# Kernel optimization log

Hardware: AMD Instinct MI355X
Metric: run time of the kernel (lower is better)

Reference implementation:

```python
import jax, jax.numpy as jnp
import numpy as np

V, D, H, L, S_MAX, FF = 32000, 1024, 16, 6, 1024, 4096
HD = D // H
EPS = 1e-5

def _ln(x, g, b):
    mu = jnp.mean(x, axis=-1, keepdims=True)
    var = jnp.mean((x - mu) ** 2, axis=-1, keepdims=True)
    return (x - mu) * jax.lax.rsqrt(var + EPS) * g + b

def setup_inputs() -> dict:
    key = jax.random.key(0)
    ks = jax.random.split(key, 12)
    std = 0.02
    d = {}
    d['x'] = jax.random.randint(ks[0], (2, 1024), 0, V)
    d['tok_emb'] = std * jax.random.normal(ks[1], (V, D), jnp.float32)
    d['pos_emb'] = std * jax.random.normal(ks[2], (S_MAX, D), jnp.float32)
    d['ln1_g'] = jnp.ones((L, D)); d['ln1_b'] = jnp.zeros((L, D))
    d['qkv_w'] = std * jax.random.normal(ks[3], (L, 3 * D, D), jnp.float32)
    d['qkv_b'] = jnp.zeros((L, 3 * D))
    d['proj_w'] = std * jax.random.normal(ks[4], (L, D, D), jnp.float32)
    d['proj_b'] = jnp.zeros((L, D))
    d['ln2_g'] = jnp.ones((L, D)); d['ln2_b'] = jnp.zeros((L, D))
    d['fc1_w'] = std * jax.random.normal(ks[5], (L, FF, D), jnp.float32)
    d['fc1_b'] = jnp.zeros((L, FF))
    d['fc2_w'] = std * jax.random.normal(ks[6], (L, D, FF), jnp.float32)
    d['fc2_b'] = jnp.zeros((L, D))
    d['lnf_g'] = jnp.ones((D,)); d['lnf_b'] = jnp.zeros((D,))
    d['head_w'] = std * jax.random.normal(ks[7], (V, D), jnp.float32)
    return d

def _gpt(x, tok_emb, pos_emb, ln1_g, ln1_b, qkv_w, qkv_b, proj_w, proj_b,
         ln2_g, ln2_b, fc1_w, fc1_b, fc2_w, fc2_b, lnf_g, lnf_b, head_w):
    B, S = x.shape
    h = tok_emb[x] + pos_emb[:S][None]  # (B,S,D)
    scale = HD ** -0.5
    causal = jnp.tril(jnp.ones((S, S), bool))
    neg_inf = jnp.finfo(h.dtype).min

    def block(h, p):
        l1g, l1b, qw, qb, pw, pb, l2g, l2b, f1w, f1b, f2w, f2b = p
        xn = _ln(h, l1g, l1b)
        qkv = xn @ qw.T + qb  # (B,S,3D)
        qkv = qkv.reshape(B, S, 3, H, HD).transpose(2, 0, 3, 1, 4)  # (3,B,H,S,HD)
        q, k, v = qkv[0], qkv[1], qkv[2]
        scores = jnp.einsum('bhqd,bhkd->bhqk', q, k) * scale
        scores = jnp.where(causal, scores, neg_inf)
        attn = jax.nn.softmax(scores, axis=-1)
        o = jnp.einsum('bhqk,bhkd->bhqd', attn, v)
        o = o.transpose(0, 2, 1, 3).reshape(B, S, D)
        h = h + (o @ pw.T + pb)
        xn = _ln(h, l2g, l2b)
        ff = jax.nn.gelu(xn @ f1w.T + f1b, approximate=False) @ f2w.T + f2b
        return h + ff, None

    params = (ln1_g, ln1_b, qkv_w, qkv_b, proj_w, proj_b,
              ln2_g, ln2_b, fc1_w, fc1_b, fc2_w, fc2_b)
    h, _ = jax.lax.scan(block, h, params)
    h = _ln(h, lnf_g, lnf_b)
    return h @ head_w.T  # (B,S,V)

def reference(x, tok_emb, pos_emb, ln1_g, ln1_b, qkv_w, qkv_b, proj_w, proj_b,
              ln2_g, ln2_b, fc1_w, fc1_b, fc2_w, fc2_b, lnf_g, lnf_b, head_w):
    return _gpt(x, tok_emb, pos_emb, ln1_g, ln1_b, qkv_w, qkv_b, proj_w, proj_b,
                ln2_g, ln2_b, fc1_w, fc1_b, fc2_w, fc2_b, lnf_g, lnf_b, head_w)
```

## Files before the change

### kernel.cpp

```cpp
#include <hip/hip_runtime.h>

typedef unsigned short u16;
typedef unsigned int   u32;
typedef __bf16 bf16x8 __attribute__((ext_vector_type(8)));
typedef float  f32x4  __attribute__((ext_vector_type(4)));

#define DEV __device__ __forceinline__

DEV u16 f2bf(float f) {
    u32 u = __builtin_bit_cast(u32, f);
    u32 r = u + 0x7FFFu + ((u >> 16) & 1u);
    return (u16)(r >> 16);
}

DEV void gload16(const void* g, void* l) {
    __builtin_amdgcn_global_load_lds((const __attribute__((address_space(1))) void*)g,
                                     (__attribute__((address_space(3))) void*)l, 16, 0, 0);
}

DEV int xcd_swz(int bid, int nwg) {
    int q = nwg >> 3, r = nwg & 7;
    int xcd = bid & 7, idx = bid >> 3;
    return (xcd < r ? xcd * (q + 1) : r * (q + 1) + (xcd - r) * q) + idx;
}

DEV int swz(int p) {
    int m = (((p >> 7) & 1) << 6) | (((p >> 9) & 1) << 5) | (((p >> 8) & 1) << 4);
    return p ^ m;
}

__global__ void cvt_k(const float* __restrict__ src, u16* __restrict__ dst, int n4) {
    int i = blockIdx.x * blockDim.x + threadIdx.x;
    int stride = gridDim.x * blockDim.x;
    for (; i < n4; i += stride) {
        float4 v = ((const float4*)src)[i];
        ushort4 u;
        u.x = f2bf(v.x); u.y = f2bf(v.y); u.z = f2bf(v.z); u.w = f2bf(v.w);
        ((ushort4*)dst)[i] = u;
    }
}

__global__ void cvt4_k(const float* __restrict__ s0, const float* __restrict__ s1,
                       const float* __restrict__ s2, const float* __restrict__ s3,
                       u16* __restrict__ dst, int n0, int n1, int n2, int n3) {
    int i = blockIdx.x * blockDim.x + threadIdx.x;
    int stride = gridDim.x * blockDim.x;
    int t0 = n0, t1 = t0 + n1, t2 = t1 + n2, t3 = t2 + n3;
    for (; i < t3; i += stride) {
        const float* s; int j;
        if (i < t0)      { s = s0; j = i; }
        else if (i < t1) { s = s1; j = i - t0; }
        else if (i < t2) { s = s2; j = i - t1; }
        else             { s = s3; j = i - t2; }
        float4 v = ((const float4*)s)[j];
        ushort4 u;
        u.x = f2bf(v.x); u.y = f2bf(v.y); u.z = f2bf(v.z); u.w = f2bf(v.w);
        ((ushort4*)dst)[i] = u;
    }
}

DEV void ln_store(float4 v, const float* __restrict__ g, const float* __restrict__ b,
                  u16* __restrict__ out, int row, int t) {
    float s = v.x + v.y + v.z + v.w;
    float s2 = v.x * v.x + v.y * v.y + v.z * v.z + v.w * v.w;
    #pragma unroll
    for (int msk = 1; msk < 64; msk <<= 1) {
        s  += __shfl_xor(s, msk);
        s2 += __shfl_xor(s2, msk);
    }
    __shared__ float ps[4], ps2[4];
    if ((t & 63) == 0) { ps[t >> 6] = s; ps2[t >> 6] = s2; }
    __syncthreads();
    s = ps[0] + ps[1] + ps[2] + ps[3];
    s2 = ps2[0] + ps2[1] + ps2[2] + ps2[3];
    float mu = s * (1.0f / 1024.0f);
    float var = s2 * (1.0f / 1024.0f) - mu * mu;
    float rstd = rsqrtf(var + 1e-5f);
    float4 gg = ((const float4*)g)[t];
    float4 bb = ((const float4*)b)[t];
    ushort4 o;
    o.x = f2bf((v.x - mu) * rstd * gg.x + bb.x);
    o.y = f2bf((v.y - mu) * rstd * gg.y + bb.y);
    o.z = f2bf((v.z - mu) * rstd * gg.z + bb.z);
    o.w = f2bf((v.w - mu) * rstd * gg.w + bb.w);
    ((ushort4*)out)[(size_t)row * 256 + t] = o;
}

__global__ void ln_k(const float* __restrict__ in, const float* __restrict__ g,
                     const float* __restrict__ b, u16* __restrict__ out) {
    int row = blockIdx.x;
    int t = threadIdx.x;
    float4 v = ((const float4*)(in + (size_t)row * 1024))[t];
    ln_store(v, g, b, out, row, t);
}

__global__ void embed_ln_k(const int* __restrict__ x, const float* __restrict__ te,
                           const float* __restrict__ pe, float* __restrict__ h,
                           const float* __restrict__ g, const float* __restrict__ b,
                           u16* __restrict__ xn) {
    int row = blockIdx.x;
    int t = threadIdx.x;
    int tok = x[row];
    int s = row & 1023;
    float4 a = ((const float4*)(te + (size_t)tok * 1024))[t];
    float4 p = ((const float4*)(pe + (size_t)s * 1024))[t];
    a.x += p.x; a.y += p.y; a.z += p.z; a.w += p.w;
    ((float4*)(h + (size_t)row * 1024))[t] = a;
    ln_store(a, g, b, xn, row, t);
}

__global__ void fuse2ln_k(const float* __restrict__ p0, const float* __restrict__ p1,
                          const float* __restrict__ bias, float* __restrict__ h,
                          const float* __restrict__ g, const float* __restrict__ b,
                          u16* __restrict__ xn) {
    int row = blockIdx.x;
    int t = threadIdx.x;
    size_t idx = (size_t)row * 256 + t;
    float4 a = ((const float4*)p0)[idx];
    float4 bb = ((const float4*)p1)[idx];
    float4 c = ((const float4*)bias)[t];
    float4 v = ((const float4*)h)[idx];
    v.x += a.x + bb.x + c.x;
    v.y += a.y + bb.y + c.y;
    v.z += a.z + bb.z + c.z;
    v.w += a.w + bb.w + c.w;
    ((float4*)h)[idx] = v;
    ln_store(v, g, b, xn, row, t);
}

template<int PH>
DEV void phase_mma(const bf16x8 (&af)[2][2], const bf16x8 (&bfr)[4][2], f32x4 (&acc)[8][4]) {
    __builtin_amdgcn_s_barrier();
    asm volatile("s_waitcnt lgkmcnt(0)" ::: "memory");
    __builtin_amdgcn_sched_barrier(0);
    __builtin_amdgcn_s_setprio(1);
    #pragma unroll
    for (int ms = 0; ms < 2; ++ms)
        #pragma unroll
        for (int nj = 0; nj < 4; ++nj)
            #pragma unroll
            for (int kk = 0; kk < 2; ++kk)
                acc[PH * 2 + ms][nj] = __builtin_amdgcn_mfma_f32_16x16x32_bf16(
                    af[ms][kk], bfr[nj][kk], acc[PH * 2 + ms][nj], 0, 0, 0);
    __builtin_amdgcn_s_setprio(0);
}

template<int PH>
DEV void read_afrags(const char* Ab, int arow, int fr, int fq, bf16x8 (&af)[2][2]) {
    #pragma unroll
    for (int ms = 0; ms < 2; ++ms)
        #pragma unroll
        for (int kk = 0; kk < 2; ++kk) {
            int lin = (arow + (PH * 2 + ms) * 16 + fr) * 128 + kk * 64 + fq * 16;
            af[ms][kk] = *(const bf16x8*)(Ab + swz(lin));
        }
}

template<int BIAS, int OUTBF>
__global__ __launch_bounds__(512, 2)
void gemm8p(const u16* __restrict__ A, const u16* __restrict__ Bw,
            const float* __restrict__ bias,
            float* __restrict__ outf, u16* __restrict__ outb,
            int M, int N, int K) {
    __shared__ char lds[131072];
    char* ldsA = lds;
    char* ldsB = lds + 65536;
    const int t = threadIdx.x;
    const int w = t >> 6, l = t & 63;
    const int fr = l & 15, fq = l >> 4;
    const int wm = w >> 2, wn = w & 3;

    int bid = blockIdx.y * gridDim.x + blockIdx.x;
    int swzb = xcd_swz(bid, gridDim.x * gridDim.y);
    const int m0 = (swzb % gridDim.x) * 256;
    const int n0 = (swzb / gridDim.x) * 256;
    const int nt = K >> 6;
    const int arow = wm * 128;

    const u16* Asrc = A + (size_t)m0 * K;
    const u16* Bsrc = Bw + (size_t)n0 * K;

    size_t o00, o01, o10, o11;
    {
        int p;
        p = 0 * 16384 + 0 * 8192 + t * 16; o00 = (size_t)(p >> 7) * K + ((swz(p) & 127) >> 1);
        p = 0 * 16384 + 1 * 8192 + t * 16; o01 = (size_t)(p >> 7) * K + ((swz(p) & 127) >> 1);
        p = 1 * 16384 + 0 * 8192 + t * 16; o10 = (size_t)(p >> 7) * K + ((swz(p) & 127) >> 1);
        p = 1 * 16384 + 1 * 8192 + t * 16; o11 = (size_t)(p >> 7) * K + ((swz(p) & 127) >> 1);
    }
    const int wb = w * 1024;

    gload16(Asrc + o00, ldsA + wb);
    gload16(Asrc + o01, ldsA + 8192 + wb);
    gload16(Asrc + o10, ldsA + 16384 + wb);
    gload16(Asrc + o11, ldsA + 16384 + 8192 + wb);
    gload16(Bsrc + o00, ldsB + wb);
    gload16(Bsrc + o01, ldsB + 8192 + wb);
    gload16(Bsrc + o10, ldsB + 16384 + wb);
    gload16(Bsrc + o11, ldsB + 16384 + 8192 + wb);
    gload16(Bsrc + o00 + 64, ldsB + 32768 + wb);
    gload16(Bsrc + o01 + 64, ldsB + 32768 + 8192 + wb);
    gload16(Bsrc + o10 + 64, ldsB + 32768 + 16384 + wb);
    gload16(Bsrc + o11 + 64, ldsB + 32768 + 16384 + 8192 + wb);
    asm volatile("s_waitcnt vmcnt(4)" ::: "memory");
    __builtin_amdgcn_s_barrier();
    __builtin_amdgcn_sched_barrier(0);

    f32x4 acc[8][4] = {};

    for (int T = 0; T < nt; ++T) {
        const char* Ab = ldsA + (T & 1) * 32768;
        const char* Bb = ldsB + (T & 1) * 32768;
        char* Anx = ldsA + ((T + 1) & 1) * 32768;
        char* Bnx = ldsB + (T & 1) * 32768;
        const bool stA = (T + 1 < nt), stB = (T + 2 < nt);
        const size_t kA = (size_t)(T + 1) * 64, kB = (size_t)(T + 2) * 64;

        bf16x8 bfr[4][2], af[2][2];

        #pragma unroll
        for (int nj = 0; nj < 4; ++nj)
            #pragma unroll
            for (int kk = 0; kk < 2; ++kk) {
                int lin = (wn * 64 + nj * 16 + fr) * 128 + kk * 64 + fq * 16;
                bfr[nj][kk] = *(const bf16x8*)(Bb + swz(lin));
            }
        read_afrags<0>(Ab, arow, fr, fq, af);
        if (stA) {
            gload16(Asrc + o00 + kA, Anx + wb);
            gload16(Asrc + o01 + kA, Anx + 8192 + wb);
        }
        phase_mma<0>(af, bfr, acc);
        __builtin_amdgcn_s_barrier();

        read_afrags<1>(Ab, arow, fr, fq, af);
        if (stA) {
            gload16(Asrc + o10 + kA, Anx + 16384 + wb);
            gload16(Asrc + o11 + kA, Anx + 16384 + 8192 + wb);
        }
        phase_mma<1>(af, bfr, acc);
        __builtin_amdgcn_s_barrier();

        read_afrags<2>(Ab, arow, fr, fq, af);
        if (stB) {
            gload16(Bsrc + o00 + kB, Bnx + wb);
            gload16(Bsrc + o01 + kB, Bnx + 8192 + wb);
        }
        phase_mma<2>(af, bfr, acc);
        __builtin_amdgcn_s_barrier();

        read_afrags<3>(Ab, arow, fr, fq, af);
        if (stB) {
            gload16(Bsrc + o10 + kB, Bnx + 16384 + wb);
            gload16(Bsrc + o11 + kB, Bnx + 16384 + 8192 + wb);
        }
        phase_mma<3>(af, bfr, acc);
        if (stB)      asm volatile("s_waitcnt vmcnt(4)" ::: "memory");
        else if (stA) asm volatile("s_waitcnt vmcnt(0)" ::: "memory");
        __builtin_amdgcn_s_barrier();
        __builtin_amdgcn_sched_barrier(0);
    }

    #pragma unroll
    for (int mi = 0; mi < 8; ++mi) {
        #pragma unroll
        for (int nj = 0; nj < 4; ++nj) {
            #pragma unroll
            for (int r = 0; r < 4; ++r) {
                int row = m0 + wm * 128 + mi * 16 + fq * 4 + r;
                int col = n0 + wn * 64 + nj * 16 + fr;
                float v = acc[mi][nj][r];
                if (BIAS) v += bias[col];
                if (OUTBF) outb[(size_t)row * N + col] = f2bf(v);
                else       outf[(size_t)row * N + col] = v;
            }
        }
    }
}

template<int BIAS, int GELU_, int OUTBF, int SPLITK>
__global__ __launch_bounds__(512, 2)
void gemm4p(const u16* __restrict__ A, const u16* __restrict__ Bw,
            const float* __restrict__ bias,
            float* __restrict__ outf, u16* __restrict__ outb,
            int M, int N, int K) {
    __shared__ char lds[65536];
    char* ldsA = lds;
    char* ldsB = lds + 32768;
    const int t = threadIdx.x;
    const int w = t >> 6, l = t & 63;
    const int fr = l & 15, fq = l >> 4;
    const int wm = w >> 2, wn = w & 3;

    int bid = blockIdx.y * gridDim.x + blockIdx.x;
    int swzb = xcd_swz(bid, gridDim.x * gridDim.y);
    const int m0 = (swzb % gridDim.x) * 128;
    const int n0 = (swzb / gridDim.x) * 128;

    int kbase = 0, Keff = K;
    if (SPLITK) { Keff = K >> 1; kbase = blockIdx.z * Keff; }
    const int nt = Keff >> 6;

    const u16* Asrc = A + (size_t)m0 * K + kbase;
    const u16* Bsrc = Bw + (size_t)n0 * K + kbase;

    size_t o0, o1;
    {
        int p = t * 16;        o0 = (size_t)(p >> 7) * K + ((swz(p) & 127) >> 1);
        p = 8192 + t * 16;     o1 = (size_t)(p >> 7) * K + ((swz(p) & 127) >> 1);
    }
    const int wb = w * 1024;

    gload16(Asrc + o0, ldsA + wb);
    gload16(Asrc + o1, ldsA + 8192 + wb);
    gload16(Bsrc + o0, ldsB + wb);
    gload16(Bsrc + o1, ldsB + 8192 + wb);
    gload16(Bsrc + o0 + 64, ldsB + 16384 + wb);
    gload16(Bsrc + o1 + 64, ldsB + 16384 + 8192 + wb);
    asm volatile("s_waitcnt vmcnt(2)" ::: "memory");
    __builtin_amdgcn_s_barrier();
    __builtin_amdgcn_sched_barrier(0);

    f32x4 acc[4][2] = {};

    for (int T = 0; T < nt; ++T) {
        const char* Ab = ldsA + (T & 1) * 16384;
        const char* Bb = ldsB + (T & 1) * 16384;
        char* Anx = ldsA + ((T + 1) & 1) * 16384;
        char* Bnx = ldsB + (T & 1) * 16384;
        const bool stA = (T + 1 < nt), stB = (T + 2 < nt);
        const size_t kA = (size_t)(T + 1) * 64, kB = (size_t)(T + 2) * 64;

        bf16x8 bfr[2][2], af[2][2];

        #pragma unroll
        for (int nj = 0; nj < 2; ++nj)
            #pragma unroll
            for (int kk = 0; kk < 2; ++kk) {
                int lin = (wn * 32 + nj * 16 + fr) * 128 + kk * 64 + fq * 16;
                bfr[nj][kk] = *(const bf16x8*)(Bb + swz(lin));
            }
        #pragma unroll
        for (int ms = 0; ms < 2; ++ms)
            #pragma unroll
            for (int kk = 0; kk < 2; ++kk) {
                int lin = (wm * 64 + ms * 16 + fr) * 128 + kk * 64 + fq * 16;
                af[ms][kk] = *(const bf16x8*)(Ab + swz(lin));
            }
        if (stA) {
            gload16(Asrc + o0 + kA, Anx + wb);
            gload16(Asrc + o1 + kA, Anx + 8192 + wb);
        }
        __builtin_amdgcn_s_barrier();
        asm volatile("s_waitcnt lgkmcnt(0)" ::: "memory");
        __builtin_amdgcn_sched_barrier(0);
        __builtin_amdgcn_s_setprio(1);
        #pragma unroll
        for (int ms = 0; ms < 2; ++ms)
            #pragma unroll
            for (int nj = 0; nj < 2; ++nj)
                #pragma unroll
                for (int kk = 0; kk < 2; ++kk)
                    acc[ms][nj] = __builtin_amdgcn_mfma_f32_16x16x32_bf16(
                        af[ms][kk], bfr[nj][kk], acc[ms][nj], 0, 0, 0);
        __builtin_amdgcn_s_setprio(0);
        __builtin_amdgcn_s_barrier();

        #pragma unroll
        for (int ms = 0; ms < 2; ++ms)
            #pragma unroll
            for (int kk = 0; kk < 2; ++kk) {
                int lin = (wm * 64 + (2 + ms) * 16 + fr) * 128 + kk * 64 + fq * 16;
                af[ms][kk] = *(const bf16x8*)(Ab + swz(lin));
            }
        if (stB) {
            gload16(Bsrc + o0 + kB, Bnx + wb);
            gload16(Bsrc + o1 + kB, Bnx + 8192 + wb);
        }
        __builtin_amdgcn_s_barrier();
        asm volatile("s_waitcnt lgkmcnt(0)" ::: "memory");
        __builtin_amdgcn_sched_barrier(0);
        __builtin_amdgcn_s_setprio(1);
        #pragma unroll
        for (int ms = 0; ms < 2; ++ms)
            #pragma unroll
            for (int nj = 0; nj < 2; ++nj)
                #pragma unroll
                for (int kk = 0; kk < 2; ++kk)
                    acc[2 + ms][nj] = __builtin_amdgcn_mfma_f32_16x16x32_bf16(
                        af[ms][kk], bfr[nj][kk], acc[2 + ms][nj], 0, 0, 0);
        __builtin_amdgcn_s_setprio(0);
        if (stB)      asm volatile("s_waitcnt vmcnt(2)" ::: "memory");
        else if (stA) asm volatile("s_waitcnt vmcnt(0)" ::: "memory");
        __builtin_amdgcn_s_barrier();
        __builtin_amdgcn_sched_barrier(0);
    }

    float* op = outf;
    if (SPLITK) op = outf + (size_t)blockIdx.z * M * N;

    #pragma unroll
    for (int mi = 0; mi < 4; ++mi) {
        #pragma unroll
        for (int nj = 0; nj < 2; ++nj) {
            #pragma unroll
            for (int r = 0; r < 4; ++r) {
                int row = m0 + wm * 64 + mi * 16 + fq * 4 + r;
                int col = n0 + wn * 32 + nj * 16 + fr;
                float v = acc[mi][nj][r];
                if (BIAS) v += bias[col];
                if (GELU_) v = 0.5f * v * (1.0f + erff(v * 0.70710678118f));
                if (OUTBF) outb[(size_t)row * N + col] = f2bf(v);
                else       op[(size_t)row * N + col] = v;
            }
        }
    }
}

template<int BM, int BN, int BIAS, int GELU_, int RES, int OUTBF, int SPLITK>
__global__ void gemm_db(const u16* __restrict__ A, const u16* __restrict__ Bw,
                        const float* __restrict__ bias, const float* __restrict__ res,
                        float* __restrict__ outf, u16* __restrict__ outb,
                        int M, int N, int K) {
    constexpr int MR = BM / 32;
    constexpr int NR = BN / 32;
    constexpr int AL = BM / 64;
    constexpr int BL = BN / 64;
    __shared__ u16 lA[2][BM * 32];
    __shared__ u16 lB[2][BN * 32];
    const int t = threadIdx.x;
    const int w = t >> 6, l = t & 63;

    int bid = blockIdx.y * gridDim.x + blockIdx.x;
    int swzb = xcd_swz(bid, gridDim.x * gridDim.y);
    const int m0 = (swzb % gridDim.x) * BM;
    const int n0 = (swzb / gridDim.x) * BN;

    int kbase = 0, Keff = K;
    if (SPLITK) { Keff = K >> 1; kbase = blockIdx.z * Keff; }
    const int nt = Keff >> 5;

    const int wr = (w >> 1) * (BM / 2), wc = (w & 1) * (BN / 2);
    const int fr = l & 15, fq = l >> 4;
    const int g0 = w * 64 + l;

    const int srow = g0 >> 2, scol = (g0 & 3) * 8;

    f32x4 acc[MR][NR] = {};

    #pragma unroll
    for (int i = 0; i < AL; ++i)
        gload16(A + (size_t)(m0 + srow + i * 64) * K + kbase + scol, lA[0] + (srow + i * 64) * 32 + scol);
    #pragma unroll
    for (int i = 0; i < BL; ++i)
        gload16(Bw + (size_t)(n0 + srow + i * 64) * K + kbase + scol, lB[0] + (srow + i * 64) * 32 + scol);
    __syncthreads();

    for (int T = 0; T < nt; ++T) {
        const int cur = T & 1, nxt = cur ^ 1;
        if (T + 1 < nt) {
            const int kk = kbase + (T + 1) * 32;
            #pragma unroll
            for (int i = 0; i < AL; ++i)
                gload16(A + (size_t)(m0 + srow + i * 64) * K + kk + scol, lA[nxt] + (srow + i * 64) * 32 + scol);
            #pragma unroll
            for (int i = 0; i < BL; ++i)
                gload16(Bw + (size_t)(n0 + srow + i * 64) * K + kk + scol, lB[nxt] + (srow + i * 64) * 32 + scol);
        }
        bf16x8 af[MR], bfv[NR];
        #pragma unroll
        for (int mi = 0; mi < MR; ++mi)
            af[mi] = *(const bf16x8*)(lA[cur] + (wr + mi * 16 + fr) * 32 + fq * 8);
        #pragma unroll
        for (int ni = 0; ni < NR; ++ni)
            bfv[ni] = *(const bf16x8*)(lB[cur] + (wc + ni * 16 + fr) * 32 + fq * 8);
        #pragma unroll
        for (int mi = 0; mi < MR; ++mi)
            #pragma unroll
            for (int ni = 0; ni < NR; ++ni)
                acc[mi][ni] = __builtin_amdgcn_mfma_f32_16x16x32_bf16(af[mi], bfv[ni], acc[mi][ni], 0, 0, 0);
        __syncthreads();
    }

    float* op = outf;
    if (SPLITK) op = outf + (size_t)blockIdx.z * M * N;

    #pragma unroll
    for (int mi = 0; mi < MR; ++mi) {
        #pragma unroll
        for (int ni = 0; ni < NR; ++ni) {
            #pragma unroll
            for (int r = 0; r < 4; ++r) {
                int row = m0 + wr + mi * 16 + fq * 4 + r;
                int col = n0 + wc + ni * 16 + fr;
                float v = acc[mi][ni][r];
                if (BIAS) v += bias[col];
                if (GELU_) v = 0.5f * v * (1.0f + erff(v * 0.70710678118f));
                if (RES) v += res[(size_t)row * N + col];
                if (OUTBF) outb[(size_t)row * N + col] = f2bf(v);
                else       op[(size_t)row * N + col] = v;
            }
        }
    }
}

__global__ __launch_bounds__(512, 2)
void attn_k(const u16* __restrict__ qkv, u16* __restrict__ o) {
    __shared__ u16 lK[64 * 64];
    __shared__ u16 lV[64 * 64];
    __shared__ u16 lP[8 * 16 * 64];
    const int t = threadIdx.x;
    const int w = t >> 6, l = t & 63;
    const int fr = l & 15, fq = l >> 4;

    int swzb = xcd_swz(blockIdx.x, gridDim.x);
    const int qb = 7 - (swzb & 7);
    const int hh = (swzb >> 3) & 15;
    const int b  = swzb >> 7;
    const int q0 = qb * 128;
    const int qw = q0 + w * 16;

    const u16* srcK;
    {
        int p = t * 16;
        int L = swz(p);
        srcK = qkv + ((size_t)(b * 1024) + (L >> 7)) * 3072 + 1024 + hh * 64 + ((L & 127) >> 1);
    }

    const int kvp = (t & 31) * 2;
    const int vd0 = (t >> 5) * 4;
    const u16* srcV = qkv + (size_t)(b * 1024) * 3072 + 2048 + hh * 64 + vd0;

    bf16x8 qf[2];
    {
        size_t base = ((size_t)(b * 1024) + qw + fr) * 3072 + hh * 64;
        qf[0] = *(const bf16x8*)(qkv + base + fq * 8);
        qf[1] = *(const bf16x8*)(qkv + base + 32 + fq * 8);
    }

    float m_run[4], l_run[4];
    f32x4 acc_o[4] = {};
    #pragma unroll
    for (int r = 0; r < 4; ++r) { m_run[r] = -__builtin_inff(); l_run[r] = 0.0f; }

    uint2 gv0 = *(const uint2*)(srcV + (size_t)kvp * 3072);
    uint2 gv1 = *(const uint2*)(srcV + (size_t)(kvp + 1) * 3072);

    const int kv_end = q0 + 128;
    for (int kv0 = 0; kv0 < kv_end; kv0 += 64) {
        #pragma unroll
        for (int j = 0; j < 4; ++j) {
            u32 lo = (j < 2) ? gv0.x : gv0.y;
            u32 hi = (j < 2) ? gv1.x : gv1.y;
            lo = (j & 1) ? (lo >> 16) : (lo & 0xffffu);
            hi = (j & 1) ? (hi >> 16) : (hi & 0xffffu);
            u32 word = lo | (hi << 16);
            int pv = (vd0 + j) * 128 + kvp * 2;
            *(u32*)((char*)lV + swz(pv)) = word;
        }
        gload16(srcK + (size_t)kv0 * 3072, (char*)lK + w * 1024);
        __syncthreads();

        if (kv0 + 64 < kv_end) {
            gv0 = *(const uint2*)(srcV + (size_t)(kv0 + 64 + kvp) * 3072);
            gv1 = *(const uint2*)(srcV + (size_t)(kv0 + 64 + kvp + 1) * 3072);
        }

        const bool active = (kv0 <= qw + 15);
        if (active) {
            f32x4 accs[4] = {};
            #pragma unroll
            for (int nt = 0; nt < 4; ++nt) {
                #pragma unroll
                for (int ks = 0; ks < 2; ++ks) {
                    int pk = ((nt * 16 + fr) * 64 + ks * 32 + fq * 8) * 2;
                    bf16x8 kf = *(const bf16x8*)((const char*)lK + swz(pk));
                    accs[nt] = __builtin_amdgcn_mfma_f32_16x16x32_bf16(qf[ks], kf, accs[nt], 0, 0, 0);
                }
            }

            float p[4][4], mx[4], rs[4];
            #pragma unroll
            for (int r = 0; r < 4; ++r) {
                int qg = qw + fq * 4 + r;
                float m = -__builtin_inff();
                #pragma unroll
                for (int nt = 0; nt < 4; ++nt) {
                    int kvg = kv0 + nt * 16 + fr;
                    float s = (kvg <= qg) ? accs[nt][r] * 0.125f : -__builtin_inff();
                    p[nt][r] = s;
                    m = fmaxf(m, s);
                }
                mx[r] = m;
            }
            #pragma unroll
            for (int msk = 1; msk < 16; msk <<= 1) {
                #pragma unroll
                for (int r = 0; r < 4; ++r) mx[r] = fmaxf(mx[r], __shfl_xor(mx[r], msk));
            }
            float mnew[4], alpha[4];
            #pragma unroll
            for (int r = 0; r < 4; ++r) {
                mnew[r] = fmaxf(m_run[r], mx[r]);
                alpha[r] = __expf(m_run[r] - mnew[r]);
                float s = 0.0f;
                #pragma unroll
                for (int nt = 0; nt < 4; ++nt) {
                    float pv = __expf(p[nt][r] - mnew[r]);
                    p[nt][r] = pv;
                    s += pv;
                }
                rs[r] = s;
            }
            #pragma unroll
            for (int msk = 1; msk < 16; msk <<= 1) {
                #pragma unroll
                for (int r = 0; r < 4; ++r) rs[r] += __shfl_xor(rs[r], msk);
            }
            #pragma unroll
            for (int r = 0; r < 4; ++r) {
                l_run[r] = l_run[r] * alpha[r] + rs[r];
                m_run[r] = mnew[r];
            }
            #pragma unroll
            for (int nt = 0; nt < 4; ++nt)
                #pragma unroll
                for (int r = 0; r < 4; ++r) acc_o[nt][r] *= alpha[r];

            #pragma unroll
            for (int nt = 0; nt < 4; ++nt)
                #pragma unroll
                for (int r = 0; r < 4; ++r) {
                    int pp = (w * 1024 + (fq * 4 + r) * 64 + nt * 16 + fr) * 2;
                    *(u16*)((char*)lP + swz(pp)) = f2bf(p[nt][r]);
                }

            bf16x8 pa[2];
            #pragma unroll
            for (int ks = 0; ks < 2; ++ks) {
                int ppr = (w * 1024 + fr * 64 + ks * 32 + fq * 8) * 2;
                pa[ks] = *(const bf16x8*)((const char*)lP + swz(ppr));
            }
            #pragma unroll
            for (int nt = 0; nt < 4; ++nt) {
                #pragma unroll
                for (int ks = 0; ks < 2; ++ks) {
                    int pvr = ((nt * 16 + fr) * 64 + ks * 32 + fq * 8) * 2;
                    bf16x8 vf = *(const bf16x8*)((const char*)lV + swz(pvr));
                    acc_o[nt] = __builtin_amdgcn_mfma_f32_16x16x32_bf16(pa[ks], vf, acc_o[nt], 0, 0, 0);
                }
            }
        }
        __syncthreads();
    }

    #pragma unroll
    for (int nt = 0; nt < 4; ++nt) {
        #pragma unroll
        for (int r = 0; r < 4; ++r) {
            int qg = qw + fq * 4 + r;
            int d = nt * 16 + fr;
            float ov = acc_o[nt][r] / l_run[r];
            o[((size_t)(b * 1024) + qg) * 1024 + hh * 64 + d] = f2bf(ov);
        }
    }
}

extern "C" void kernel_launch(void* const* d_in, const int* in_sizes, int n_in,
                              void* d_out, int out_size, void* d_ws, size_t ws_size,
                              hipStream_t stream) {
    const int*   x       = (const int*)  d_in[0];
    const float* tok_emb = (const float*)d_in[1];
    const float* pos_emb = (const float*)d_in[2];
    const float* ln1_g   = (const float*)d_in[3];
    const float* ln1_b   = (const float*)d_in[4];
    const float* qkv_w   = (const float*)d_in[5];
    const float* qkv_b   = (const float*)d_in[6];
    const float* proj_w  = (const float*)d_in[7];
    const float* proj_b  = (const float*)d_in[8];
    const float* ln2_g   = (const float*)d_in[9];
    const float* ln2_b   = (const float*)d_in[10];
    const float* fc1_w   = (const float*)d_in[11];
    const float* fc1_b   = (const float*)d_in[12];
    const float* fc2_w   = (const float*)d_in[13];
    const float* fc2_b   = (const float*)d_in[14];
    const float* lnf_g   = (const float*)d_in[15];
    const float* lnf_b   = (const float*)d_in[16];
    const float* head_w  = (const float*)d_in[17];
    float* out = (float*)d_out;

    char* ws = (char*)d_ws;
    float* h   = (float*)(ws + 0);
    u16*   xn  = (u16*)(ws + 8388608);
    u16*   qkv = (u16*)(ws + 12582912);
    u16*   ob  = (u16*)(ws + 25165824);
    u16*   ff  = (u16*)(ws + 29360128);
    u16*   wq  = (u16*)(ws + 46137344);
    float* pbuf = (float*)(ws + 12582912);

    u16* wqkv = wq;
    u16* wproj = wqkv + 3072 * 1024;
    u16* wfc1  = wproj + 1024 * 1024;
    u16* wfc2  = wfc1 + 4096 * 1024;

    const int M = 2048;

    embed_ln_k<<<dim3(2048), 256, 0, stream>>>(x, tok_emb, pos_emb, h, ln1_g, ln1_b, xn);

    for (int lyr = 0; lyr < 6; ++lyr) {
        cvt4_k<<<dim3(2048), 256, 0, stream>>>(
            qkv_w + (size_t)lyr * 3072 * 1024, proj_w + (size_t)lyr * 1024 * 1024,
            fc1_w + (size_t)lyr * 4096 * 1024, fc2_w + (size_t)lyr * 1024 * 4096,
            wq, 3072 * 256, 1024 * 256, 4096 * 256, 4096 * 256);
        gemm4p<1, 0, 1, 0><<<dim3(16, 24), 512, 0, stream>>>(
            xn, wqkv, qkv_b + lyr * 3072, nullptr, qkv, M, 3072, 1024);
        attn_k<<<dim3(256), 512, 0, stream>>>(qkv, ob);
        gemm_db<64, 64, 1, 0, 1, 0, 0><<<dim3(32, 16), 256, 0, stream>>>(
            ob, wproj, proj_b + lyr * 1024, h, h, nullptr, M, 1024, 1024);
        ln_k<<<dim3(2048), 256, 0, stream>>>(h, ln2_g + lyr * 1024, ln2_b + lyr * 1024, xn);
        gemm4p<1, 1, 1, 0><<<dim3(16, 32), 512, 0, stream>>>(
            xn, wfc1, fc1_b + lyr * 4096, nullptr, ff, M, 4096, 1024);
        gemm4p<0, 0, 0, 1><<<dim3(16, 8, 2), 512, 0, stream>>>(
            ff, wfc2, nullptr, pbuf, nullptr, M, 1024, 4096);
        const float* g = (lyr < 5) ? (ln1_g + (lyr + 1) * 1024) : lnf_g;
        const float* b = (lyr < 5) ? (ln1_b + (lyr + 1) * 1024) : lnf_b;
        fuse2ln_k<<<dim3(2048), 256, 0, stream>>>(
            pbuf, pbuf + (size_t)M * 1024, fc2_b + lyr * 1024, h, g, b, xn);
    }

    cvt_k<<<dim3(2048), 256, 0, stream>>>(head_w, wq, 32000 * 1024 / 4);
    gemm8p<0, 0><<<dim3(8, 125), 512, 0, stream>>>(
        xn, wq, nullptr, out, nullptr, M, 32000, 1024);
}
```

Baseline: 1.205 ms.

## Fuse fp32-to-bf16 weight conversion into GEMM B-tile loads

The per-layer conversion of QKV, FC1 and FC2 weights to bf16 is removed. The GEMM now reads fp32 weights through registers, packs them to bf16 and writes them to LDS, with a register-staged prefetch one tile ahead; the B buffer indexing changes to match. This avoids a separate conversion kernel that writes and rereads about 12M bf16 weights per layer. In exchange the GEMM moves twice the bytes for B from global memory and does extra conversion ALU work and LDS writes inside the main loop.

```diff
diff --git a/kernel.cpp b/kernel.cpp
--- a/kernel.cpp
+++ b/kernel.cpp
@@ -27,6 +27,15 @@
 DEV int swz(int p) {
     int m = (((p >> 7) & 1) << 6) | (((p >> 9) & 1) << 5) | (((p >> 8) & 1) << 4);
     return p ^ m;
+}
+
+DEV void packwrite16(float4 a, float4 b, char* dst) {
+    uint4 v;
+    v.x = (u32)f2bf(a.x) | ((u32)f2bf(a.y) << 16);
+    v.y = (u32)f2bf(a.z) | ((u32)f2bf(a.w) << 16);
+    v.z = (u32)f2bf(b.x) | ((u32)f2bf(b.y) << 16);
+    v.w = (u32)f2bf(b.z) | ((u32)f2bf(b.w) << 16);
+    *(uint4*)dst = v;
 }
 
 __global__ void cvt_k(const float* __restrict__ src, u16* __restrict__ dst, int n4) {
@@ -34,25 +43,6 @@
     int stride = gridDim.x * blockDim.x;
     for (; i < n4; i += stride) {
         float4 v = ((const float4*)src)[i];
-        ushort4 u;
-        u.x = f2bf(v.x); u.y = f2bf(v.y); u.z = f2bf(v.z); u.w = f2bf(v.w);
-        ((ushort4*)dst)[i] = u;
-    }
-}
-
-__global__ void cvt4_k(const float* __restrict__ s0, const float* __restrict__ s1,
-                       const float* __restrict__ s2, const float* __restrict__ s3,
-                       u16* __restrict__ dst, int n0, int n1, int n2, int n3) {
-    int i = blockIdx.x * blockDim.x + threadIdx.x;
-    int stride = gridDim.x * blockDim.x;
-    int t0 = n0, t1 = t0 + n1, t2 = t1 + n2, t3 = t2 + n3;
-    for (; i < t3; i += stride) {
-        const float* s; int j;
-        if (i < t0)      { s = s0; j = i; }
-        else if (i < t1) { s = s1; j = i - t0; }
-        else if (i < t2) { s = s2; j = i - t1; }
-        else             { s = s3; j = i - t2; }
-        float4 v = ((const float4*)s)[j];
         ushort4 u;
         u.x = f2bf(v.x); u.y = f2bf(v.y); u.z = f2bf(v.z); u.w = f2bf(v.w);
         ((ushort4*)dst)[i] = u;
@@ -280,10 +270,10 @@
 
 template<int BIAS, int GELU_, int OUTBF, int SPLITK>
 __global__ __launch_bounds__(512, 2)
-void gemm4p(const u16* __restrict__ A, const u16* __restrict__ Bw,
-            const float* __restrict__ bias,
-            float* __restrict__ outf, u16* __restrict__ outb,
-            int M, int N, int K) {
+void gemm4pf(const u16* __restrict__ A, const float* __restrict__ Bw32,
+             const float* __restrict__ bias,
+             float* __restrict__ outf, u16* __restrict__ outb,
+             int M, int N, int K) {
     __shared__ char lds[65536];
     char* ldsA = lds;
     char* ldsB = lds + 32768;
@@ -302,7 +292,6 @@
     const int nt = Keff >> 6;
 
     const u16* Asrc = A + (size_t)m0 * K + kbase;
-    const u16* Bsrc = Bw + (size_t)n0 * K + kbase;
 
     size_t o0, o1;
     {
@@ -311,13 +300,25 @@
     }
     const int wb = w * 1024;
 
+    const int p0 = t * 16, p1 = 8192 + t * 16;
+    const int q0s = swz(p0), q1s = swz(p1);
+    const float* Bs0 = Bw32 + (size_t)(n0 + (p0 >> 7)) * K + kbase + ((p0 & 127) >> 1);
+    const float* Bs1 = Bw32 + (size_t)(n0 + (p1 >> 7)) * K + kbase + ((p1 & 127) >> 1);
+
+    float4 rb0, rb1, rb2, rb3;
+
+    rb0 = *(const float4*)(Bs0);     rb1 = *(const float4*)(Bs0 + 4);
+    rb2 = *(const float4*)(Bs1);     rb3 = *(const float4*)(Bs1 + 4);
     gload16(Asrc + o0, ldsA + wb);
     gload16(Asrc + o1, ldsA + 8192 + wb);
-    gload16(Bsrc + o0, ldsB + wb);
-    gload16(Bsrc + o1, ldsB + 8192 + wb);
-    gload16(Bsrc + o0 + 64, ldsB + 16384 + wb);
-    gload16(Bsrc + o1 + 64, ldsB + 16384 + 8192 + wb);
     asm volatile("s_waitcnt vmcnt(2)" ::: "memory");
+    packwrite16(rb0, rb1, ldsB + q0s);
+    packwrite16(rb2, rb3, ldsB + q1s);
+    if (nt > 1) {
+        rb0 = *(const float4*)(Bs0 + 64);  rb1 = *(const float4*)(Bs0 + 68);
+        rb2 = *(const float4*)(Bs1 + 64);  rb3 = *(const float4*)(Bs1 + 68);
+    }
+    asm volatile("s_waitcnt vmcnt(4) lgkmcnt(0)" ::: "memory");
     __builtin_amdgcn_s_barrier();
     __builtin_amdgcn_sched_barrier(0);
 
@@ -327,9 +328,10 @@
         const char* Ab = ldsA + (T & 1) * 16384;
         const char* Bb = ldsB + (T & 1) * 16384;
         char* Anx = ldsA + ((T + 1) & 1) * 16384;
-        char* Bnx = ldsB + (T & 1) * 16384;
+        char* Bnx = ldsB + ((T + 1) & 1) * 16384;
         const bool stA = (T + 1 < nt), stB = (T + 2 < nt);
-        const size_t kA = (size_t)(T + 1) * 64, kB = (size_t)(T + 2) * 64;
+        const size_t kA = (size_t)(T + 1) * 64;
+        const size_t kB = (size_t)(T + 2) * 64;
 
         bf16x8 bfr[2][2], af[2][2];
 
@@ -373,9 +375,14 @@
                 int lin = (wm * 64 + (2 + ms) * 16 + fr) * 128 + kk * 64 + fq * 16;
                 af[ms][kk] = *(const bf16x8*)(Ab + swz(lin));
             }
-        if (stB) {
-            gload16(Bsrc + o0 + kB, Bnx + wb);
-            gload16(Bsrc + o1 + kB, Bnx + 8192 + wb);
+        if (stA) {
+            asm volatile("s_waitcnt vmcnt(2)" ::: "memory");
+            packwrite16(rb0, rb1, Bnx + q0s);
+            packwrite16(rb2, rb3, Bnx + q1s);
+            if (stB) {
+                rb0 = *(const float4*)(Bs0 + kB);      rb1 = *(const float4*)(Bs0 + kB + 4);
+                rb2 = *(const float4*)(Bs1 + kB);      rb3 = *(const float4*)(Bs1 + kB + 4);
+            }
         }
         __builtin_amdgcn_s_barrier();
         asm volatile("s_waitcnt lgkmcnt(0)" ::: "memory");
@@ -390,7 +397,7 @@
                     acc[2 + ms][nj] = __builtin_amdgcn_mfma_f32_16x16x32_bf16(
                         af[ms][kk], bfr[nj][kk], acc[2 + ms][nj], 0, 0, 0);
         __builtin_amdgcn_s_setprio(0);
-        if (stB)      asm volatile("s_waitcnt vmcnt(2)" ::: "memory");
+        if (stB)      asm volatile("s_waitcnt vmcnt(4)" ::: "memory");
         else if (stA) asm volatile("s_waitcnt vmcnt(0)" ::: "memory");
         __builtin_amdgcn_s_barrier();
         __builtin_amdgcn_sched_barrier(0);
@@ -698,30 +705,22 @@
     u16*   wq  = (u16*)(ws + 46137344);
     float* pbuf = (float*)(ws + 12582912);
 
-    u16* wqkv = wq;
-    u16* wproj = wqkv + 3072 * 1024;
-    u16* wfc1  = wproj + 1024 * 1024;
-    u16* wfc2  = wfc1 + 4096 * 1024;
-
     const int M = 2048;
 
     embed_ln_k<<<dim3(2048), 256, 0, stream>>>(x, tok_emb, pos_emb, h, ln1_g, ln1_b, xn);
 
     for (int lyr = 0; lyr < 6; ++lyr) {
-        cvt4_k<<<dim3(2048), 256, 0, stream>>>(
-            qkv_w + (size_t)lyr * 3072 * 1024, proj_w + (size_t)lyr * 1024 * 1024,
-            fc1_w + (size_t)lyr * 4096 * 1024, fc2_w + (size_t)lyr * 1024 * 4096,
-            wq, 3072 * 256, 1024 * 256, 4096 * 256, 4096 * 256);
-        gemm4p<1, 0, 1, 0><<<dim3(16, 24), 512, 0, stream>>>(
-            xn, wqkv, qkv_b + lyr * 3072, nullptr, qkv, M, 3072, 1024);
+        cvt_k<<<dim3(512), 256, 0, stream>>>(proj_w + (size_t)lyr * 1024 * 1024, wq, 1024 * 1024 / 4);
+        gemm4pf<1, 0, 1, 0><<<dim3(16, 24), 512, 0, stream>>>(
+            xn, qkv_w + (size_t)lyr * 3072 * 1024, qkv_b + lyr * 3072, nullptr, qkv, M, 3072, 1024);
         attn_k<<<dim3(256), 512, 0, stream>>>(qkv, ob);
         gemm_db<64, 64, 1, 0, 1, 0, 0><<<dim3(32, 16), 256, 0, stream>>>(
-            ob, wproj, proj_b + lyr * 1024, h, h, nullptr, M, 1024, 1024);
+            ob, wq, proj_b + lyr * 1024, h, h, nullptr, M, 1024, 1024);
         ln_k<<<dim3(2048), 256, 0, stream>>>(h, ln2_g + lyr * 1024, ln2_b + lyr * 1024, xn);
-        gemm4p<1, 1, 1, 0><<<dim3(16, 32), 512, 0, stream>>>(
-            xn, wfc1, fc1_b + lyr * 4096, nullptr, ff, M, 4096, 1024);
-        gemm4p<0, 0, 0, 1><<<dim3(16, 8, 2), 512, 0, stream>>>(
-            ff, wfc2, nullptr, pbuf, nullptr, M, 1024, 4096);
+        gemm4pf<1, 1, 1, 0><<<dim3(16, 32), 512, 0, stream>>>(
+            xn, fc1_w + (size_t)lyr * 4096 * 1024, fc1_b + lyr * 4096, nullptr, ff, M, 4096, 1024);
+        gemm4pf<0, 0, 0, 1><<<dim3(16, 8, 2), 512, 0, stream>>>(
+            ff, fc2_w + (size_t)lyr * 1024 * 4096, nullptr, pbuf, nullptr, M, 1024, 4096);
         const float* g = (lyr < 5) ? (ln1_g + (lyr + 1) * 1024) : lnf_g;
         const float* b = (lyr < 5) ? (ln1_b + (lyr + 1) * 1024) : lnf_b;
         fuse2ln_k<<<dim3(2048), 256, 0, stream>>>(
```

New measurement: 1.274 ms. +5.7%, slower.

## Double-buffer K/V tiles in attention and skip softmax rescale when max barely changes

Applied to the files above, without the earlier changes.

The attention kernel now keeps two LDS buffers for K and V. It prefetches the next tile's K via async global-to-LDS load and stores the next V after compute, which removes one __syncthreads per iteration and overlaps loads with MFMA work. It also adds a lazy-rescale path: when no row max rises more than 8 above the running max, it reuses the stale max and skips the alpha rescale of the accumulator. This doubles K/V LDS use, which may cut occupancy, and keeps exp values bounded by e^8 rather than 1 in the fast path.

```diff
diff --git a/kernel.cpp b/kernel.cpp
--- a/kernel.cpp
+++ b/kernel.cpp
@@ -506,8 +506,8 @@
 
 __global__ __launch_bounds__(512, 2)
 void attn_k(const u16* __restrict__ qkv, u16* __restrict__ o) {
-    __shared__ u16 lK[64 * 64];
-    __shared__ u16 lV[64 * 64];
+    __shared__ u16 lK[2][64 * 64];
+    __shared__ u16 lV[2][64 * 64];
     __shared__ u16 lP[8 * 16 * 64];
     const int t = threadIdx.x;
     const int w = t >> 6, l = t & 63;
@@ -545,23 +545,26 @@
 
     uint2 gv0 = *(const uint2*)(srcV + (size_t)kvp * 3072);
     uint2 gv1 = *(const uint2*)(srcV + (size_t)(kvp + 1) * 3072);
+    gload16(srcK, (char*)lK[0] + w * 1024);
+    #pragma unroll
+    for (int j = 0; j < 4; ++j) {
+        u32 lo = (j < 2) ? gv0.x : gv0.y;
+        u32 hi = (j < 2) ? gv1.x : gv1.y;
+        lo = (j & 1) ? (lo >> 16) : (lo & 0xffffu);
+        hi = (j & 1) ? (hi >> 16) : (hi & 0xffffu);
+        u32 word = lo | (hi << 16);
+        int pv = (vd0 + j) * 128 + kvp * 2;
+        *(u32*)((char*)lV[0] + swz(pv)) = word;
+    }
 
     const int kv_end = q0 + 128;
-    for (int kv0 = 0; kv0 < kv_end; kv0 += 64) {
-        #pragma unroll
-        for (int j = 0; j < 4; ++j) {
-            u32 lo = (j < 2) ? gv0.x : gv0.y;
-            u32 hi = (j < 2) ? gv1.x : gv1.y;
-            lo = (j & 1) ? (lo >> 16) : (lo & 0xffffu);
-            hi = (j & 1) ? (hi >> 16) : (hi & 0xffffu);
-            u32 word = lo | (hi << 16);
-            int pv = (vd0 + j) * 128 + kvp * 2;
-            *(u32*)((char*)lV + swz(pv)) = word;
-        }
-        gload16(srcK + (size_t)kv0 * 3072, (char*)lK + w * 1024);
+    int cur = 0;
+    for (int kv0 = 0; kv0 < kv_end; kv0 += 64, cur ^= 1) {
         __syncthreads();
-
-        if (kv0 + 64 < kv_end) {
+        const int nxt = cur ^ 1;
+        const bool more = (kv0 + 64 < kv_end);
+        if (more) {
+            gload16(srcK + (size_t)(kv0 + 64) * 3072, (char*)lK[nxt] + w * 1024);
             gv0 = *(const uint2*)(srcV + (size_t)(kv0 + 64 + kvp) * 3072);
             gv1 = *(const uint2*)(srcV + (size_t)(kv0 + 64 + kvp + 1) * 3072);
         }
@@ -574,7 +577,7 @@
                 #pragma unroll
                 for (int ks = 0; ks < 2; ++ks) {
                     int pk = ((nt * 16 + fr) * 64 + ks * 32 + fq * 8) * 2;
-                    bf16x8 kf = *(const bf16x8*)((const char*)lK + swz(pk));
+                    bf16x8 kf = *(const bf16x8*)((const char*)lK[cur] + swz(pk));
                     accs[nt] = __builtin_amdgcn_mfma_f32_16x16x32_bf16(qf[ks], kf, accs[nt], 0, 0, 0);
                 }
             }
@@ -598,34 +601,59 @@
                 #pragma unroll
                 for (int r = 0; r < 4; ++r) mx[r] = fmaxf(mx[r], __shfl_xor(mx[r], msk));
             }
-            float mnew[4], alpha[4];
-            #pragma unroll
-            for (int r = 0; r < 4; ++r) {
-                mnew[r] = fmaxf(m_run[r], mx[r]);
-                alpha[r] = __expf(m_run[r] - mnew[r]);
-                float s = 0.0f;
-                #pragma unroll
-                for (int nt = 0; nt < 4; ++nt) {
-                    float pv = __expf(p[nt][r] - mnew[r]);
-                    p[nt][r] = pv;
-                    s += pv;
-                }
-                rs[r] = s;
-            }
-            #pragma unroll
-            for (int msk = 1; msk < 16; msk <<= 1) {
-                #pragma unroll
-                for (int r = 0; r < 4; ++r) rs[r] += __shfl_xor(rs[r], msk);
-            }
-            #pragma unroll
-            for (int r = 0; r < 4; ++r) {
-                l_run[r] = l_run[r] * alpha[r] + rs[r];
-                m_run[r] = mnew[r];
-            }
-            #pragma unroll
-            for (int nt = 0; nt < 4; ++nt)
-                #pragma unroll
-                for (int r = 0; r < 4; ++r) acc_o[nt][r] *= alpha[r];
+
+            bool need = false;
+            #pragma unroll
+            for (int r = 0; r < 4; ++r) need |= (mx[r] > m_run[r] + 8.0f);
+            if (__any(need)) {
+                float mnew[4], alpha[4];
+                #pragma unroll
+                for (int r = 0; r < 4; ++r) {
+                    mnew[r] = fmaxf(m_run[r], mx[r]);
+                    alpha[r] = __expf(m_run[r] - mnew[r]);
+                    float s = 0.0f;
+                    #pragma unroll
+                    for (int nt = 0; nt < 4; ++nt) {
+                        float pv = __expf(p[nt][r] - mnew[r]);
+                        p[nt][r] = pv;
+                        s += pv;
+                    }
+                    rs[r] = s;
+                }
+                #pragma unroll
+                for (int msk = 1; msk < 16; msk <<= 1) {
+                    #pragma unroll
+                    for (int r = 0; r < 4; ++r) rs[r] += __shfl_xor(rs[r], msk);
+                }
+                #pragma unroll
+                for (int r = 0; r < 4; ++r) {
+                    l_run[r] = l_run[r] * alpha[r] + rs[r];
+                    m_run[r] = mnew[r];
+                }
+                #pragma unroll
+                for (int nt = 0; nt < 4; ++nt)
+                    #pragma unroll
+                    for (int r = 0; r < 4; ++r) acc_o[nt][r] *= alpha[r];
+            } else {
+                #pragma unroll
+                for (int r = 0; r < 4; ++r) {
+                    float s = 0.0f;
+                    #pragma unroll
+                    for (int nt = 0; nt < 4; ++nt) {
+                        float pv = __expf(p[nt][r] - m_run[r]);
+                        p[nt][r] = pv;
+                        s += pv;
+                    }
+                    rs[r] = s;
+                }
+                #pragma unroll
+                for (int msk = 1; msk < 16; msk <<= 1) {
+                    #pragma unroll
+                    for (int r = 0; r < 4; ++r) rs[r] += __shfl_xor(rs[r], msk);
+                }
+                #pragma unroll
+                for (int r = 0; r < 4; ++r) l_run[r] += rs[r];
+            }
 
             #pragma unroll
             for (int nt = 0; nt < 4; ++nt)
@@ -646,12 +674,24 @@
                 #pragma unroll
                 for (int ks = 0; ks < 2; ++ks) {
                     int pvr = ((nt * 16 + fr) * 64 + ks * 32 + fq * 8) * 2;
-                    bf16x8 vf = *(const bf16x8*)((const char*)lV + swz(pvr));
+                    bf16x8 vf = *(const bf16x8*)((const char*)lV[cur] + swz(pvr));
                     acc_o[nt] = __builtin_amdgcn_mfma_f32_16x16x32_bf16(pa[ks], vf, acc_o[nt], 0, 0, 0);
                 }
             }
         }
-        __syncthreads();
+
+        if (more) {
+            #pragma unroll
+            for (int j = 0; j < 4; ++j) {
+                u32 lo = (j < 2) ? gv0.x : gv0.y;
+                u32 hi = (j < 2) ? gv1.x : gv1.y;
+                lo = (j & 1) ? (lo >> 16) : (lo & 0xffffu);
+                hi = (j & 1) ? (hi >> 16) : (hi & 0xffffu);
+                u32 word = lo | (hi << 16);
+                int pv = (vd0 + j) * 128 + kvp * 2;
+                *(u32*)((char*)lV[nxt] + swz(pv)) = word;
+            }
+        }
     }
 
     #pragma unroll
```

New measurement: 1.193 ms (median of 2 runs). Within noise of the previous version (-1.0%).
